# Optimization experiments

Measured on AMD Instinct MI355X. Metric: run time of the kernel, lower is better.

Reference implementation:

```python
import jax, jax.numpy as jnp
import numpy as np

NUM_INPUTS = 4096
K = 64
BATCH = 16384


def setup_inputs() -> dict:
    key = jax.random.key(0)
    X = jax.random.normal(key, (BATCH, NUM_INPUTS), dtype=jnp.float32)
    return {"X": X}


def reference(X):
    # Per-row (1 - k/n) quantile of |X| (linear interpolation, matching
    # torch.quantile default), then soft-threshold preserving sign.
    q = 1.0 - K / NUM_INPUTS
    X_abs = jnp.abs(X)
    Q = jnp.quantile(X_abs, q, axis=1, method="linear")  # [batch]
    X_trunc = jnp.maximum(X_abs - Q[:, None], 0.0)
    return jnp.sign(X) * X_trunc
```

## Files before the change

### kernel.cpp

```cpp
#include <hip/hip_runtime.h>
#include <cstdint>

constexpr int NCOLS   = 4096;
constexpr int THREADS = 256;
constexpr int EPT     = NCOLS / THREADS;
constexpr int KSEL    = 65;

__device__ __forceinline__ float soft(float x, float Q) {
    float r = fmaxf(fabsf(x) - Q, 0.0f);
    return copysignf(r, x);
}

__global__ __launch_bounds__(THREADS) void topk_sparsify(
    const float* __restrict__ X, float* __restrict__ out, int rows)
{
    const int row = blockIdx.x;
    if (row >= rows) return;
    const int t = threadIdx.x;

    const float4* __restrict__ x4 = reinterpret_cast<const float4*>(X + (size_t)row * NCOLS);
    float4* __restrict__       o4 = reinterpret_cast<float4*>(out + (size_t)row * NCOLS);

    float4 d[4];
#pragma unroll
    for (int i = 0; i < 4; ++i) d[i] = x4[t + THREADS * i];

    uint32_t a[EPT];
#pragma unroll
    for (int i = 0; i < 4; ++i) {
        a[4*i+0] = __float_as_uint(d[i].x) & 0x7FFFFFFFu;
        a[4*i+1] = __float_as_uint(d[i].y) & 0x7FFFFFFFu;
        a[4*i+2] = __float_as_uint(d[i].z) & 0x7FFFFFFFu;
        a[4*i+3] = __float_as_uint(d[i].w) & 0x7FFFFFFFu;
    }

    __shared__ uint32_t hist[2048];
    __shared__ uint32_t scan[THREADS];
    __shared__ uint32_t sel_digit_s;
    __shared__ uint32_t sel_k_s;
    __shared__ uint32_t wcnt[4], wmn[4];
    __shared__ float    q_sh;

    uint32_t known = 0;
    uint32_t k     = KSEL;

    const int      shifts[3] = {20, 10, 0};
    const uint32_t dmask [3] = {0x7FFu, 0x3FFu, 0x3FFu};
    const int      nbins [3] = {2048, 1024, 1024};
    const uint32_t pmask [3] = {0u, 0xFFF00000u, 0xFFFFFC00u};

#pragma unroll
    for (int p = 0; p < 3; ++p) {
        const int      sh = shifts[p];
        const uint32_t dm = dmask[p];
        const int      nb = nbins[p];
        const uint32_t pm = pmask[p];

        for (int b = t; b < nb; b += THREADS) hist[b] = 0u;
        __syncthreads();

#pragma unroll
        for (int i = 0; i < EPT; ++i) {
            if ((a[i] & pm) == known) {
                atomicAdd(&hist[(a[i] >> sh) & dm], 1u);
            }
        }
        __syncthreads();

        const int gpb  = nb / THREADS;
        const int base = t * gpb;
        uint32_t gsum = 0;
        for (int j = 0; j < gpb; ++j) gsum += hist[base + j];
        scan[t] = gsum;
        __syncthreads();

        for (int off = 1; off < THREADS; off <<= 1) {
            uint32_t val = scan[t];
            if (t + off < THREADS) val += scan[t + off];
            __syncthreads();
            scan[t] = val;
            __syncthreads();
        }
        const uint32_t above = (t + 1 < THREADS) ? scan[t + 1] : 0u;

        uint32_t G = above;
        for (int j = gpb - 1; j >= 0; --j) {
            const uint32_t c = hist[base + j];
            if (G < k && k <= G + c) {
                sel_digit_s = (uint32_t)(base + j);
                sel_k_s     = k - G;
            }
            G += c;
        }
        __syncthreads();
        known |= sel_digit_s << sh;
        k = sel_k_s;
        __syncthreads();
    }

    const uint32_t b65 = known;
    const float    v65 = __uint_as_float(b65);

    uint32_t cnt = 0, mn = 0xFFFFFFFFu;
#pragma unroll
    for (int i = 0; i < EPT; ++i) {
        if (a[i] > b65) { cnt++; mn = min(mn, a[i]); }
    }
#pragma unroll
    for (int off = 32; off >= 1; off >>= 1) {
        cnt += __shfl_down(cnt, off, 64);
        uint32_t m2 = __shfl_down(mn, off, 64);
        mn = min(mn, m2);
    }
    const int wave = t >> 6, lane = t & 63;
    if (lane == 0) { wcnt[wave] = cnt; wmn[wave] = mn; }
    __syncthreads();
    if (t == 0) {
        uint32_t C = wcnt[0] + wcnt[1] + wcnt[2] + wcnt[3];
        uint32_t M = min(min(wmn[0], wmn[1]), min(wmn[2], wmn[3]));
        float v64 = (C == 64u) ? __uint_as_float(M) : v65;
        q_sh = fmaf(0.015625f, v64 - v65, v65);
    }
    __syncthreads();
    const float Q = q_sh;

#pragma unroll
    for (int i = 0; i < 4; ++i) {
        float4 f = d[i];
        f.x = soft(f.x, Q);
        f.y = soft(f.y, Q);
        f.z = soft(f.z, Q);
        f.w = soft(f.w, Q);
        o4[t + THREADS * i] = f;
    }
}

extern "C" void kernel_launch(void* const* d_in, const int* in_sizes, int n_in,
                              void* d_out, int out_size, void* d_ws, size_t ws_size,
                              hipStream_t stream) {
    const float* X  = (const float*)d_in[0];
    float*       out = (float*)d_out;
    const int rows = in_sizes[0] / NCOLS;
    topk_sparsify<<<rows, THREADS, 0, stream>>>(X, out, rows);
}
```

Before: 439.0 us.

## Replace radix histogram select with prefilter-compaction and ballot bitwise select

Before selecting, each row counts the values above a fixed threshold (|x| > 2.0). If that count lies between 65 and 256, the candidates are compacted into shared memory and a single wave finds the 65th-largest value by bitwise binary search with ballots. Otherwise it falls back to a block-wide bitwise search using shuffle reductions. This replaces three histogram passes, each with shared atomics and a block scan, which carried many barriers. Global loads and stores become nontemporal. The fast path depends on the input distribution (normal data gives about 93 values above 2 per row), and the fallback costs 31 barrier rounds.

Result: faster. 411.8 us (-6.2%).

```diff
diff --git a/kernel.cpp b/kernel.cpp
--- a/kernel.cpp
+++ b/kernel.cpp
@@ -5,6 +5,10 @@
 constexpr int THREADS = 256;
 constexpr int EPT     = NCOLS / THREADS;
 constexpr int KSEL    = 65;
+constexpr uint32_t TPAT = 0x40000000u;
+constexpr int CAP     = 256;
+
+typedef float f32x4 __attribute__((ext_vector_type(4)));
 
 __device__ __forceinline__ float soft(float x, float Q) {
     float r = fmaxf(fabsf(x) - Q, 0.0f);
@@ -16,109 +20,121 @@
 {
     const int row = blockIdx.x;
     if (row >= rows) return;
-    const int t = threadIdx.x;
+    const int t    = threadIdx.x;
+    const int lane = t & 63;
+    const int wave = t >> 6;
 
-    const float4* __restrict__ x4 = reinterpret_cast<const float4*>(X + (size_t)row * NCOLS);
-    float4* __restrict__       o4 = reinterpret_cast<float4*>(out + (size_t)row * NCOLS);
+    const f32x4* __restrict__ x4 = reinterpret_cast<const f32x4*>(X + (size_t)row * NCOLS);
+    f32x4* __restrict__       o4 = reinterpret_cast<f32x4*>(out + (size_t)row * NCOLS);
 
-    float4 d[4];
+    f32x4 d[4];
 #pragma unroll
-    for (int i = 0; i < 4; ++i) d[i] = x4[t + THREADS * i];
+    for (int i = 0; i < 4; ++i) d[i] = __builtin_nontemporal_load(x4 + t + THREADS * i);
 
     uint32_t a[EPT];
 #pragma unroll
     for (int i = 0; i < 4; ++i) {
-        a[4*i+0] = __float_as_uint(d[i].x) & 0x7FFFFFFFu;
-        a[4*i+1] = __float_as_uint(d[i].y) & 0x7FFFFFFFu;
-        a[4*i+2] = __float_as_uint(d[i].z) & 0x7FFFFFFFu;
-        a[4*i+3] = __float_as_uint(d[i].w) & 0x7FFFFFFFu;
+#pragma unroll
+        for (int j = 0; j < 4; ++j)
+            a[4 * i + j] = __float_as_uint(d[i][j]) & 0x7FFFFFFFu;
     }
 
-    __shared__ uint32_t hist[2048];
-    __shared__ uint32_t scan[THREADS];
-    __shared__ uint32_t sel_digit_s;
-    __shared__ uint32_t sel_k_s;
+    __shared__ uint32_t list[CAP];
+    __shared__ uint32_t wtot[4];
     __shared__ uint32_t wcnt[4], wmn[4];
+    __shared__ uint32_t b65_s;
     __shared__ float    q_sh;
 
-    uint32_t known = 0;
-    uint32_t k     = KSEL;
+    uint32_t cnt = 0;
+#pragma unroll
+    for (int i = 0; i < EPT; ++i) cnt += (a[i] > TPAT) ? 1u : 0u;
 
-    const int      shifts[3] = {20, 10, 0};
-    const uint32_t dmask [3] = {0x7FFu, 0x3FFu, 0x3FFu};
-    const int      nbins [3] = {2048, 1024, 1024};
-    const uint32_t pmask [3] = {0u, 0xFFF00000u, 0xFFFFFC00u};
+    uint32_t inc = cnt;
+#pragma unroll
+    for (int off = 1; off < 64; off <<= 1) {
+        uint32_t v = __shfl_up(inc, off, 64);
+        if (lane >= off) inc += v;
+    }
+    if (lane == 63) wtot[wave] = inc;
+    __syncthreads();
 
+    uint32_t C = 0, base = 0;
 #pragma unroll
-    for (int p = 0; p < 3; ++p) {
-        const int      sh = shifts[p];
-        const uint32_t dm = dmask[p];
-        const int      nb = nbins[p];
-        const uint32_t pm = pmask[p];
+    for (int w = 0; w < 4; ++w) {
+        uint32_t tw = wtot[w];
+        C += tw;
+        if (w < wave) base += tw;
+    }
+    const bool fast = (C >= (uint32_t)KSEL) && (C <= (uint32_t)CAP);
 
-        for (int b = t; b < nb; b += THREADS) hist[b] = 0u;
-        __syncthreads();
+    if (fast) {
+        uint32_t o = base + inc - cnt;
+#pragma unroll
+        for (int i = 0; i < EPT; ++i)
+            if (a[i] > TPAT) list[o++] = a[i];
+    }
+    __syncthreads();
 
-#pragma unroll
-        for (int i = 0; i < EPT; ++i) {
-            if ((a[i] & pm) == known) {
-                atomicAdd(&hist[(a[i] >> sh) & dm], 1u);
+    uint32_t b65;
+    if (fast) {
+        if (t < 64) {
+            const uint32_t c0 = ((uint32_t)t        < C) ? list[t]        : 0u;
+            const uint32_t c1 = ((uint32_t)t + 64u  < C) ? list[t + 64]   : 0u;
+            const uint32_t c2 = ((uint32_t)t + 128u < C) ? list[t + 128]  : 0u;
+            const uint32_t c3 = ((uint32_t)t + 192u < C) ? list[t + 192]  : 0u;
+            uint32_t prefix = 0, kk = KSEL;
+            for (int b = 30; b >= 0; --b) {
+                const uint32_t want = prefix | (1u << b);
+                const uint32_t mhi  = ~((1u << b) - 1u);
+                uint64_t m0 = __ballot((c0 & mhi) == want);
+                uint64_t m1 = __ballot((c1 & mhi) == want);
+                uint64_t m2 = __ballot((c2 & mhi) == want);
+                uint64_t m3 = __ballot((c3 & mhi) == want);
+                const uint32_t cc = (uint32_t)(__popcll(m0) + __popcll(m1) +
+                                               __popcll(m2) + __popcll(m3));
+                if (cc >= kk) prefix = want; else kk -= cc;
             }
+            if (t == 0) b65_s = prefix;
         }
         __syncthreads();
-
-        const int gpb  = nb / THREADS;
-        const int base = t * gpb;
-        uint32_t gsum = 0;
-        for (int j = 0; j < gpb; ++j) gsum += hist[base + j];
-        scan[t] = gsum;
-        __syncthreads();
-
-        for (int off = 1; off < THREADS; off <<= 1) {
-            uint32_t val = scan[t];
-            if (t + off < THREADS) val += scan[t + off];
+        b65 = b65_s;
+    } else {
+        uint32_t prefix = 0, kk = KSEL;
+        for (int b = 30; b >= 0; --b) {
+            const uint32_t want = prefix | (1u << b);
+            const uint32_t mhi  = ~((1u << b) - 1u);
+            uint32_t c = 0;
+#pragma unroll
+            for (int i = 0; i < EPT; ++i) c += ((a[i] & mhi) == want) ? 1u : 0u;
+#pragma unroll
+            for (int off2 = 32; off2 >= 1; off2 >>= 1) c += __shfl_down(c, off2, 64);
+            if (lane == 0) wcnt[wave] = c;
             __syncthreads();
-            scan[t] = val;
+            const uint32_t tot = wcnt[0] + wcnt[1] + wcnt[2] + wcnt[3];
+            if (tot >= kk) prefix = want; else kk -= tot;
             __syncthreads();
         }
-        const uint32_t above = (t + 1 < THREADS) ? scan[t + 1] : 0u;
+        b65 = prefix;
+    }
+    const float v65 = __uint_as_float(b65);
 
-        uint32_t G = above;
-        for (int j = gpb - 1; j >= 0; --j) {
-            const uint32_t c = hist[base + j];
-            if (G < k && k <= G + c) {
-                sel_digit_s = (uint32_t)(base + j);
-                sel_k_s     = k - G;
-            }
-            G += c;
-        }
-        __syncthreads();
-        known |= sel_digit_s << sh;
-        k = sel_k_s;
-        __syncthreads();
-    }
-
-    const uint32_t b65 = known;
-    const float    v65 = __uint_as_float(b65);
-
-    uint32_t cnt = 0, mn = 0xFFFFFFFFu;
+    uint32_t cgt = 0, mn = 0xFFFFFFFFu;
 #pragma unroll
     for (int i = 0; i < EPT; ++i) {
-        if (a[i] > b65) { cnt++; mn = min(mn, a[i]); }
+        if (a[i] > b65) { cgt++; mn = min(mn, a[i]); }
     }
 #pragma unroll
-    for (int off = 32; off >= 1; off >>= 1) {
-        cnt += __shfl_down(cnt, off, 64);
-        uint32_t m2 = __shfl_down(mn, off, 64);
+    for (int off2 = 32; off2 >= 1; off2 >>= 1) {
+        cgt += __shfl_down(cgt, off2, 64);
+        uint32_t m2 = __shfl_down(mn, off2, 64);
         mn = min(mn, m2);
     }
-    const int wave = t >> 6, lane = t & 63;
-    if (lane == 0) { wcnt[wave] = cnt; wmn[wave] = mn; }
+    if (lane == 0) { wcnt[wave] = cgt; wmn[wave] = mn; }
     __syncthreads();
     if (t == 0) {
-        uint32_t C = wcnt[0] + wcnt[1] + wcnt[2] + wcnt[3];
-        uint32_t M = min(min(wmn[0], wmn[1]), min(wmn[2], wmn[3]));
-        float v64 = (C == 64u) ? __uint_as_float(M) : v65;
+        const uint32_t Ct = wcnt[0] + wcnt[1] + wcnt[2] + wcnt[3];
+        const uint32_t M  = min(min(wmn[0], wmn[1]), min(wmn[2], wmn[3]));
+        const float v64 = (Ct == 64u) ? __uint_as_float(M) : v65;
         q_sh = fmaf(0.015625f, v64 - v65, v65);
     }
     __syncthreads();
@@ -126,19 +142,17 @@
 
 #pragma unroll
     for (int i = 0; i < 4; ++i) {
-        float4 f = d[i];
-        f.x = soft(f.x, Q);
-        f.y = soft(f.y, Q);
-        f.z = soft(f.z, Q);
-        f.w = soft(f.w, Q);
-        o4[t + THREADS * i] = f;
+        f32x4 f;
+#pragma unroll
+        for (int j = 0; j < 4; ++j) f[j] = soft(d[i][j], Q);
+        __builtin_nontemporal_store(f, o4 + t + THREADS * i);
     }
 }
 
 extern "C" void kernel_launch(void* const* d_in, const int* in_sizes, int n_in,
                               void* d_out, int out_size, void* d_ws, size_t ws_size,
                               hipStream_t stream) {
-    const float* X  = (const float*)d_in[0];
+    const float* X   = (const float*)d_in[0];
     float*       out = (float*)d_out;
     const int rows = in_sizes[0] / NCOLS;
     topk_sparsify<<<rows, THREADS, 0, stream>>>(X, out, rows);
```
